# Performance work log

Measured on AMD Instinct MI355X. Metric: run time of the kernel, lower is better.

The kernel has to match this reference:

```python
import jax, jax.numpy as jnp
import numpy as np

B, S, D, H = 2, 2048, 1024, 16
DK = D // H
THETA = 10000.0


def _freqs_cos_sin(dim, seq_len, theta=THETA):
    # matches precompute_freqs_cis: freqs over full d_model, pairs of adjacent dims
    inv = 1.0 / theta ** (np.arange(0, dim, 2)[: dim // 2].astype(np.float32) / dim)
    t = np.arange(seq_len, dtype=np.float32)
    ang = np.outer(t, inv)  # [S, D/2]
    return jnp.asarray(np.cos(ang)), jnp.asarray(np.sin(ang))


def setup_inputs() -> dict:
    key = jax.random.key(0)
    ks = jax.random.split(key, 11)
    sc = 1.0 / np.sqrt(D)
    cos, sin = _freqs_cos_sin(D, S)
    return {
        "query": jax.random.normal(ks[0], (B, S, D), jnp.float32),
        "key": jax.random.normal(ks[1], (B, S, D), jnp.float32),
        "value": jax.random.normal(ks[2], (B, S, D), jnp.float32),
        "wq": jax.random.normal(ks[3], (D, D), jnp.float32) * sc,
        "bq": jnp.zeros((D,), jnp.float32),
        "wk": jax.random.normal(ks[4], (D, D), jnp.float32) * sc,
        "bk": jnp.zeros((D,), jnp.float32),
        "wv": jax.random.normal(ks[5], (D, D), jnp.float32) * sc,
        "bv": jnp.zeros((D,), jnp.float32),
        "wo": jax.random.normal(ks[6], (D, D), jnp.float32) * sc,
        "bo": jnp.zeros((D,), jnp.float32),
        "cos": cos,  # [S, D/2]
        "sin": sin,  # [S, D/2]
    }


def _rope(x, cos, sin):
    # x: [B,S,D]; pairs are adjacent elements along D (view_as_complex semantics)
    xr = x.reshape(*x.shape[:-1], -1, 2)  # [B,S,D/2,2]
    x0, x1 = xr[..., 0], xr[..., 1]
    c, s = cos[None], sin[None]  # broadcast over batch
    o0 = x0 * c - x1 * s
    o1 = x0 * s + x1 * c
    return jnp.stack([o0, o1], axis=-1).reshape(x.shape)


def reference(query, key, value, wq, bq, wk, bk, wv, bv, wo, bo, cos, sin):
    q = query @ wq.T + bq
    k = key @ wk.T + bk
    v = value @ wv.T + bv
    q = _rope(q, cos, sin)
    k = _rope(k, cos, sin)
    # split heads: [B,S,D] -> [B,H,S,DK]
    q = q.reshape(B, S, H, DK).transpose(0, 2, 1, 3)
    k = k.reshape(B, S, H, DK).transpose(0, 2, 1, 3)
    v = v.reshape(B, S, H, DK).transpose(0, 2, 1, 3)
    scores = jnp.einsum("bhqd,bhkd->bhqk", q, k) / jnp.sqrt(jnp.float32(DK))
    attn = jax.nn.softmax(scores, axis=-1)  # dropout is identity in eval
    out = jnp.einsum("bhqk,bhkd->bhqd", attn, v)
    out = out.transpose(0, 2, 1, 3).reshape(B, S, D)
    return out @ wo.T + bo
```

## Files before the change

kernel.cpp:

```cpp
#include <hip/hip_runtime.h>
#include <hip/hip_fp16.h>

typedef _Float16 f16;
using f16x8 = __attribute__((ext_vector_type(8))) _Float16;
using h2 = __attribute__((ext_vector_type(2))) __fp16;
using f32x4 = __attribute__((ext_vector_type(4))) float;
using f32x16 = __attribute__((ext_vector_type(16))) float;

#define LOG2E 1.4426950408889634f

__device__ __forceinline__ void gload16(const void* g, void* l) {
  __builtin_amdgcn_global_load_lds(
      (const __attribute__((address_space(1))) void*)g,
      (__attribute__((address_space(3))) void*)l, 16, 0, 0);
}

__device__ __forceinline__ float b32(h2 x) { return __builtin_bit_cast(float, x); }
__device__ __forceinline__ unsigned u32(h2 x) { return __builtin_bit_cast(unsigned, x); }

__global__ __launch_bounds__(256) void convert_k(
    const float* __restrict__ q, const float* __restrict__ k, const float* __restrict__ v,
    const float* __restrict__ wq, const float* __restrict__ wk,
    const float* __restrict__ wv, const float* __restrict__ wo,
    f16* __restrict__ dst) {
  const size_t SEG = (size_t)4 * 1024 * 1024;
  size_t i = ((size_t)blockIdx.x * 256 + threadIdx.x) * 8;
  const float* src; size_t off;
  if (i < SEG)            { src = q;  off = i; }
  else if (i < 2 * SEG)   { src = k;  off = i - SEG; }
  else if (i < 3 * SEG)   { src = v;  off = i - 2 * SEG; }
  else {
    size_t wi = i - 3 * SEG;
    int s = (int)(wi >> 20);
    src = (s == 0) ? wq : (s == 1) ? wk : (s == 2) ? wv : wo;
    off = wi & ((1u << 20) - 1);
  }
  float4 a = *(const float4*)(src + off);
  float4 b = *(const float4*)(src + off + 4);
  f16x8 o;
  o[0] = (f16)a.x; o[1] = (f16)a.y; o[2] = (f16)a.z; o[3] = (f16)a.w;
  o[4] = (f16)b.x; o[5] = (f16)b.y; o[6] = (f16)b.z; o[7] = (f16)b.w;
  *(f16x8*)(dst + i) = o;
}

template <int QKV>
__global__ __launch_bounds__(256) void gemm_k(
    const f16* __restrict__ Abase, const f16* __restrict__ Wbase,
    const float* __restrict__ b0, const float* __restrict__ b1, const float* __restrict__ b2,
    const float* __restrict__ cosT, const float* __restrict__ sinT,
    f16* __restrict__ qh, f16* __restrict__ kh, f16* __restrict__ vt,
    float* __restrict__ outF) {
  __shared__ f16 As[2][128 * 32];
  __shared__ f16 Bs[2][128 * 32];
  int tid = threadIdx.x, wid = tid >> 6, lane = tid & 63;
  int z = QKV ? blockIdx.z : 0;
  const f16* A = Abase + (size_t)z * (4u * 1024 * 1024);
  const f16* W = Wbase + (size_t)z * (1024u * 1024);
  int m0 = blockIdx.y * 128, n0 = blockIdx.x * 128;
  int wr = wid >> 1, wc = wid & 1;
  f32x4 acc[4][4] = {};

  int srow = tid >> 2;
  int sslot = (tid & 3) ^ (srow & 3);
  const f16* asrc0 = A + (size_t)(m0 + srow) * 1024 + sslot * 8;
  const f16* asrc1 = A + (size_t)(m0 + 64 + srow) * 1024 + sslot * 8;
  const f16* bsrc0 = W + (size_t)(n0 + srow) * 1024 + sslot * 8;
  const f16* bsrc1 = W + (size_t)(n0 + 64 + srow) * 1024 + sslot * 8;

  int aoff[4], boff[4];
#pragma unroll
  for (int i = 0; i < 4; ++i) {
    int row = wr * 64 + i * 16 + (lane & 15);
    aoff[i] = row * 32 + (((lane >> 4) ^ (row & 3)) * 8);
    int col = wc * 64 + i * 16 + (lane & 15);
    boff[i] = col * 32 + (((lane >> 4) ^ (col & 3)) * 8);
  }

  gload16(asrc0, (void*)(&As[0][0] + wid * 512));
  gload16(asrc1, (void*)(&As[0][0] + 2048 + wid * 512));
  gload16(bsrc0, (void*)(&Bs[0][0] + wid * 512));
  gload16(bsrc1, (void*)(&Bs[0][0] + 2048 + wid * 512));
  __syncthreads();

  int cur = 0;
  for (int kt = 0; kt < 32; ++kt) {
    if (kt + 1 < 32) {
      int k0 = (kt + 1) * 32;
      gload16(asrc0 + k0, (void*)(&As[cur ^ 1][0] + wid * 512));
      gload16(asrc1 + k0, (void*)(&As[cur ^ 1][0] + 2048 + wid * 512));
      gload16(bsrc0 + k0, (void*)(&Bs[cur ^ 1][0] + wid * 512));
      gload16(bsrc1 + k0, (void*)(&Bs[cur ^ 1][0] + 2048 + wid * 512));
    }
    f16x8 af[4], bf[4];
#pragma unroll
    for (int i = 0; i < 4; ++i) {
      af[i] = *(const f16x8*)(&As[cur][0] + aoff[i]);
      bf[i] = *(const f16x8*)(&Bs[cur][0] + boff[i]);
    }
#pragma unroll
    for (int i = 0; i < 4; ++i)
#pragma unroll
      for (int j = 0; j < 4; ++j)
        acc[i][j] = __builtin_amdgcn_mfma_f32_16x16x32_f16(af[i], bf[j], acc[i][j], 0, 0, 0);
    __syncthreads();
    cur ^= 1;
  }

  const float* bias = QKV ? (z == 0 ? b0 : (z == 1 ? b1 : b2)) : b0;
#pragma unroll
  for (int i = 0; i < 4; ++i) {
#pragma unroll
    for (int j = 0; j < 4; ++j) {
#pragma unroll
      for (int r = 0; r < 4; ++r) {
        int grow = m0 + wr * 64 + i * 16 + ((lane >> 4) << 2) + r;
        int gcol = n0 + wc * 64 + j * 16 + (lane & 15);
        float val = acc[i][j][r] + bias[gcol];
        if (QKV) {
          int s = grow & 2047, bb = grow >> 11;
          int h = gcol >> 6, dk = gcol & 63;
          if (z < 2) {
            float pr = __shfl_xor(val, 1);
            int j2 = gcol >> 1;
            float c = cosT[s * 512 + j2], sn = sinT[s * 512 + j2];
            val = (lane & 1) ? (c * val + sn * pr) : (c * val - sn * pr);
            if (z == 0) val *= 0.125f * LOG2E;
            f16* dst = (z == 0) ? qh : kh;
            dst[(((size_t)bb * 16 + h) * 2048 + s) * 64 + dk] = (f16)val;
          } else {
            vt[(((size_t)bb * 16 + h) * 64 + dk) * 2048 + s] = (f16)val;
          }
        } else {
          outF[(size_t)grow * 1024 + gcol] = val;
        }
      }
    }
  }
}

__global__ __launch_bounds__(256, 4) void flash_k(
    const f16* __restrict__ qh, const f16* __restrict__ kh, const f16* __restrict__ vt,
    f16* __restrict__ op, float2* __restrict__ mlbuf) {
  __shared__ f16 Ks[2][64 * 64];
  __shared__ f16 Vs[2][64 * 64];
  int tid = threadIdx.x, wid = tid >> 6, lane = tid & 63;
  int l31 = lane & 31, hi = lane >> 5;
  int qt = blockIdx.x, h = blockIdx.y, z = blockIdx.z;
  int b = z >> 1, ks = z & 1;
  size_t bh = (size_t)b * 16 + h;
  const f16* qp = qh + bh * (2048 * 64);
  const f16* kp = kh + bh * (2048 * 64) + (size_t)ks * 1024 * 64;
  const f16* vp = vt + bh * (64 * 2048) + ks * 1024;
  int qrow = qt * 128 + wid * 32 + l31;

  f16x8 qf[4];
#pragma unroll
  for (int kk = 0; kk < 4; ++kk)
    qf[kk] = *(const f16x8*)(qp + (size_t)qrow * 64 + kk * 16 + hi * 8);

  int srowA = tid >> 3, srowB = srowA + 32;
  int schA = (tid & 7) ^ (srowA & 7);
  int schB = (tid & 7) ^ (srowB & 7);
  const f16* ksrcA = kp + (size_t)srowA * 64 + schA * 8;
  const f16* ksrcB = kp + (size_t)srowB * 64 + schB * 8;
  const f16* vsrcA = vp + (size_t)srowA * 2048 + schA * 8;
  const f16* vsrcB = vp + (size_t)srowB * 2048 + schB * 8;

  int offr[2][4];
#pragma unroll
  for (int kb = 0; kb < 2; ++kb)
#pragma unroll
    for (int kk = 0; kk < 4; ++kk) {
      int row = kb * 32 + l31;
      offr[kb][kk] = (row * 128 + kk * 32 + hi * 16) ^ ((row & 7) << 4);
    }

  float m_ = -1e30f, l_ = 0.f;
  f32x16 oacc[2] = {};

  gload16(ksrcA, (char*)&Ks[0][0] + tid * 16);
  gload16(ksrcB, (char*)&Ks[0][0] + 4096 + tid * 16);
  gload16(vsrcA, (char*)&Vs[0][0] + tid * 16);
  gload16(vsrcB, (char*)&Vs[0][0] + 4096 + tid * 16);
  __syncthreads();

  int cur = 0;
  for (int kt = 0; kt < 16; ++kt) {
    if (kt + 1 < 16) {
      gload16(ksrcA + (size_t)(kt + 1) * 4096, (char*)&Ks[cur ^ 1][0] + tid * 16);
      gload16(ksrcB + (size_t)(kt + 1) * 4096, (char*)&Ks[cur ^ 1][0] + 4096 + tid * 16);
      gload16(vsrcA + (size_t)(kt + 1) * 64, (char*)&Vs[cur ^ 1][0] + tid * 16);
      gload16(vsrcB + (size_t)(kt + 1) * 64, (char*)&Vs[cur ^ 1][0] + 4096 + tid * 16);
    }

    const char* kbase = (const char*)&Ks[cur][0];
    f32x16 sacc[2] = {};
#pragma unroll
    for (int kb = 0; kb < 2; ++kb)
#pragma unroll
      for (int kk = 0; kk < 4; ++kk) {
        f16x8 af = *(const f16x8*)(kbase + offr[kb][kk]);
        sacc[kb] = __builtin_amdgcn_mfma_f32_32x32x16_f16(af, qf[kk], sacc[kb], 0, 0, 0);
      }

    float t16[16];
#pragma unroll
    for (int i = 0; i < 16; ++i) t16[i] = fmaxf(sacc[0][i], sacc[1][i]);
#pragma unroll
    for (int s = 8; s; s >>= 1)
#pragma unroll
      for (int i = 0; i < s; ++i) t16[i] = fmaxf(t16[i], t16[i + s]);
    float pmax = fmaxf(t16[0], __shfl_xor(t16[0], 32));

    if (!__all(pmax <= m_ + 8.0f)) {
      float mn = fmaxf(m_, pmax);
      float al = __builtin_amdgcn_exp2f(m_ - mn);
      m_ = mn;
      l_ *= al;
#pragma unroll
      for (int mb = 0; mb < 2; ++mb)
#pragma unroll
        for (int i = 0; i < 16; ++i) oacc[mb][i] *= al;
    }

#pragma unroll
    for (int kb = 0; kb < 2; ++kb)
#pragma unroll
      for (int i = 0; i < 16; ++i)
        sacc[kb][i] = __builtin_amdgcn_exp2f(sacc[kb][i] - m_);
#pragma unroll
    for (int i = 0; i < 16; ++i) t16[i] = sacc[0][i] + sacc[1][i];
#pragma unroll
    for (int s = 8; s; s >>= 1)
#pragma unroll
      for (int i = 0; i < s; ++i) t16[i] += t16[i + s];
    l_ += t16[0] + __shfl_xor(t16[0], 32);

    f16x8 pa[4];
#pragma unroll
    for (int kk = 0; kk < 4; ++kk) {
      int kb = kk >> 1, c8 = (kk & 1) * 8;
      float wA = b32(__builtin_amdgcn_cvt_pkrtz(sacc[kb][c8 + 0], sacc[kb][c8 + 1]));
      float wB = b32(__builtin_amdgcn_cvt_pkrtz(sacc[kb][c8 + 2], sacc[kb][c8 + 3]));
      float wC = b32(__builtin_amdgcn_cvt_pkrtz(sacc[kb][c8 + 4], sacc[kb][c8 + 5]));
      float wD = b32(__builtin_amdgcn_cvt_pkrtz(sacc[kb][c8 + 6], sacc[kb][c8 + 7]));
      float oA = __shfl_xor(wA, 32), oB = __shfl_xor(wB, 32);
      float oC = __shfl_xor(wC, 32), oD = __shfl_xor(wD, 32);
      float4 ff;
      ff.x = hi ? oC : wA;
      ff.y = hi ? oD : wB;
      ff.z = hi ? wC : oA;
      ff.w = hi ? wD : oB;
      pa[kk] = __builtin_bit_cast(f16x8, ff);
    }

    const char* vbase = (const char*)&Vs[cur][0];
#pragma unroll
    for (int kk = 0; kk < 4; ++kk)
#pragma unroll
      for (int mb = 0; mb < 2; ++mb) {
        f16x8 av = *(const f16x8*)(vbase + offr[mb][kk]);
        oacc[mb] = __builtin_amdgcn_mfma_f32_32x32x16_f16(av, pa[kk], oacc[mb], 0, 0, 0);
      }

    __syncthreads();
    cur ^= 1;
  }

  float inv = 1.f / l_;
  f16* orow = op + (((size_t)z * 16 + h) * 2048 + qrow) * 64;
#pragma unroll
  for (int mb = 0; mb < 2; ++mb)
#pragma unroll
    for (int g = 0; g < 4; ++g) {
      uint2 st;
      st.x = u32(__builtin_amdgcn_cvt_pkrtz(oacc[mb][4 * g + 0] * inv, oacc[mb][4 * g + 1] * inv));
      st.y = u32(__builtin_amdgcn_cvt_pkrtz(oacc[mb][4 * g + 2] * inv, oacc[mb][4 * g + 3] * inv));
      *(uint2*)(orow + mb * 32 + g * 8 + hi * 4) = st;
    }
  if (hi == 0)
    mlbuf[((size_t)z * 16 + h) * 2048 + qrow] = make_float2(m_, l_);
}

__global__ __launch_bounds__(256) void combine_k(
    const f16* __restrict__ op, const float2* __restrict__ ml, f16* __restrict__ attnout) {
  int t = blockIdx.x * 256 + threadIdx.x;
  int row = t >> 3, c8 = t & 7;
  int b = row >> 15, h = (row >> 11) & 15, qrow = row & 2047;
  size_t i0 = ((size_t)(b * 2 + 0) * 16 + h) * 2048 + qrow;
  size_t i1 = ((size_t)(b * 2 + 1) * 16 + h) * 2048 + qrow;
  float2 a = ml[i0], c = ml[i1];
  float M = fmaxf(a.x, c.x);
  float w1 = a.y * __builtin_amdgcn_exp2f(a.x - M);
  float w2 = c.y * __builtin_amdgcn_exp2f(c.x - M);
  float inv = 1.f / (w1 + w2);
  w1 *= inv; w2 *= inv;
  f16x8 o1 = *(const f16x8*)(op + i0 * 64 + c8 * 8);
  f16x8 o2 = *(const f16x8*)(op + i1 * 64 + c8 * 8);
  f16x8 o;
#pragma unroll
  for (int e = 0; e < 8; ++e)
    o[e] = (f16)(w1 * (float)o1[e] + w2 * (float)o2[e]);
  *(f16x8*)(attnout + ((size_t)b * 2048 + qrow) * 1024 + h * 64 + c8 * 8) = o;
}

extern "C" void kernel_launch(void* const* d_in, const int* in_sizes, int n_in,
                              void* d_out, int out_size, void* d_ws, size_t ws_size,
                              hipStream_t stream) {
  (void)in_sizes; (void)n_in; (void)out_size; (void)ws_size;
  const float* query = (const float*)d_in[0];
  const float* key   = (const float*)d_in[1];
  const float* value = (const float*)d_in[2];
  const float* wq = (const float*)d_in[3];
  const float* bq = (const float*)d_in[4];
  const float* wk = (const float*)d_in[5];
  const float* bk = (const float*)d_in[6];
  const float* wv = (const float*)d_in[7];
  const float* bv = (const float*)d_in[8];
  const float* wo = (const float*)d_in[9];
  const float* bo = (const float*)d_in[10];
  const float* cosT = (const float*)d_in[11];
  const float* sinT = (const float*)d_in[12];
  float* out = (float*)d_out;
  f16* ws = (f16*)d_ws;
  const size_t SEG = (size_t)4 * 1024 * 1024;
  f16* Xh = ws;
  f16* Wh = ws + 3 * SEG;
  f16* qh = ws + 16u * 1024 * 1024;
  f16* kh = qh + SEG;
  f16* vt = kh + SEG;
  f16* attnout = ws;
  f16* op = ws + SEG;
  float2* mlb = (float2*)(ws + 12u * 1024 * 1024);

  convert_k<<<8192, 256, 0, stream>>>(query, key, value, wq, wk, wv, wo, ws);
  gemm_k<1><<<dim3(8, 32, 3), 256, 0, stream>>>(Xh, Wh, bq, bk, bv, cosT, sinT,
                                                qh, kh, vt, nullptr);
  flash_k<<<dim3(16, 16, 4), 256, 0, stream>>>(qh, kh, vt, op, mlb);
  combine_k<<<2048, 256, 0, stream>>>(op, mlb, attnout);
  gemm_k<0><<<dim3(8, 32, 1), 256, 0, stream>>>(attnout, Wh + 3u * 1024 * 1024, bo,
                                                nullptr, nullptr, nullptr, nullptr,
                                                nullptr, nullptr, nullptr, out);
}
```

Before: 170.4 us.

## Stage QKV GEMM epilogue through LDS for coalesced stores and remap blocks per XCD

The QKV epilogue now writes the rotated, biased fp16 results into a swizzled shared-memory tile, then writes whole 16-byte rows for Q/K and transposed 16-byte runs for V^T, in place of the old scattered 2-byte stores. Block indices are also remapped so that consecutive blocks on each XCD share nearby row tiles, aiming for better L2 reuse of A and W. The two staging buffers are merged into one array so the tile can be reused for the epilogue. This adds an extra barrier and LDS traffic, and the remap assumes the grid is 8 wide by 32 tall.

```diff
diff --git a/kernel.cpp b/kernel.cpp
--- a/kernel.cpp
+++ b/kernel.cpp
@@ -50,13 +50,16 @@
     const float* __restrict__ cosT, const float* __restrict__ sinT,
     f16* __restrict__ qh, f16* __restrict__ kh, f16* __restrict__ vt,
     float* __restrict__ outF) {
-  __shared__ f16 As[2][128 * 32];
-  __shared__ f16 Bs[2][128 * 32];
+  __shared__ f16 sm[4][128 * 32];
   int tid = threadIdx.x, wid = tid >> 6, lane = tid & 63;
   int z = QKV ? blockIdx.z : 0;
   const f16* A = Abase + (size_t)z * (4u * 1024 * 1024);
   const f16* W = Wbase + (size_t)z * (1024u * 1024);
-  int m0 = blockIdx.y * 128, n0 = blockIdx.x * 128;
+
+  int lid = blockIdx.x + (blockIdx.y << 3);
+  int xcd = lid & 7, q = lid >> 3;
+  int m0 = (xcd * 4 + (q & 3)) * 128;
+  int n0 = (q >> 2) * 128;
   int wr = wid >> 1, wc = wid & 1;
   f32x4 acc[4][4] = {};
 
@@ -76,26 +79,26 @@
     boff[i] = col * 32 + (((lane >> 4) ^ (col & 3)) * 8);
   }
 
-  gload16(asrc0, (void*)(&As[0][0] + wid * 512));
-  gload16(asrc1, (void*)(&As[0][0] + 2048 + wid * 512));
-  gload16(bsrc0, (void*)(&Bs[0][0] + wid * 512));
-  gload16(bsrc1, (void*)(&Bs[0][0] + 2048 + wid * 512));
+  gload16(asrc0, (void*)(&sm[0][0] + wid * 512));
+  gload16(asrc1, (void*)(&sm[0][0] + 2048 + wid * 512));
+  gload16(bsrc0, (void*)(&sm[2][0] + wid * 512));
+  gload16(bsrc1, (void*)(&sm[2][0] + 2048 + wid * 512));
   __syncthreads();
 
   int cur = 0;
   for (int kt = 0; kt < 32; ++kt) {
     if (kt + 1 < 32) {
       int k0 = (kt + 1) * 32;
-      gload16(asrc0 + k0, (void*)(&As[cur ^ 1][0] + wid * 512));
-      gload16(asrc1 + k0, (void*)(&As[cur ^ 1][0] + 2048 + wid * 512));
-      gload16(bsrc0 + k0, (void*)(&Bs[cur ^ 1][0] + wid * 512));
-      gload16(bsrc1 + k0, (void*)(&Bs[cur ^ 1][0] + 2048 + wid * 512));
+      gload16(asrc0 + k0, (void*)(&sm[cur ^ 1][0] + wid * 512));
+      gload16(asrc1 + k0, (void*)(&sm[cur ^ 1][0] + 2048 + wid * 512));
+      gload16(bsrc0 + k0, (void*)(&sm[2 + (cur ^ 1)][0] + wid * 512));
+      gload16(bsrc1 + k0, (void*)(&sm[2 + (cur ^ 1)][0] + 2048 + wid * 512));
     }
     f16x8 af[4], bf[4];
 #pragma unroll
     for (int i = 0; i < 4; ++i) {
-      af[i] = *(const f16x8*)(&As[cur][0] + aoff[i]);
-      bf[i] = *(const f16x8*)(&Bs[cur][0] + boff[i]);
+      af[i] = *(const f16x8*)(&sm[cur][0] + aoff[i]);
+      bf[i] = *(const f16x8*)(&sm[2 + cur][0] + boff[i]);
     }
 #pragma unroll
     for (int i = 0; i < 4; ++i)
@@ -107,31 +110,69 @@
   }
 
   const float* bias = QKV ? (z == 0 ? b0 : (z == 1 ? b1 : b2)) : b0;
-#pragma unroll
-  for (int i = 0; i < 4; ++i) {
-#pragma unroll
-    for (int j = 0; j < 4; ++j) {
-#pragma unroll
-      for (int r = 0; r < 4; ++r) {
-        int grow = m0 + wr * 64 + i * 16 + ((lane >> 4) << 2) + r;
-        int gcol = n0 + wc * 64 + j * 16 + (lane & 15);
-        float val = acc[i][j][r] + bias[gcol];
-        if (QKV) {
-          int s = grow & 2047, bb = grow >> 11;
-          int h = gcol >> 6, dk = gcol & 63;
+
+  if (QKV) {
+    f16* Ct = &sm[0][0];
+#pragma unroll
+    for (int i = 0; i < 4; ++i) {
+#pragma unroll
+      for (int j = 0; j < 4; ++j) {
+#pragma unroll
+        for (int r = 0; r < 4; ++r) {
+          int row_l = wr * 64 + i * 16 + ((lane >> 4) << 2) + r;
+          int col_l = wc * 64 + j * 16 + (lane & 15);
+          int gcol = n0 + col_l;
+          float val = acc[i][j][r] + bias[gcol];
           if (z < 2) {
+            int s = (m0 + row_l) & 2047;
             float pr = __shfl_xor(val, 1);
             int j2 = gcol >> 1;
             float c = cosT[s * 512 + j2], sn = sinT[s * 512 + j2];
             val = (lane & 1) ? (c * val + sn * pr) : (c * val - sn * pr);
             if (z == 0) val *= 0.125f * LOG2E;
-            f16* dst = (z == 0) ? qh : kh;
-            dst[(((size_t)bb * 16 + h) * 2048 + s) * 64 + dk] = (f16)val;
-          } else {
-            vt[(((size_t)bb * 16 + h) * 64 + dk) * 2048 + s] = (f16)val;
           }
-        } else {
-          outF[(size_t)grow * 1024 + gcol] = val;
+          Ct[row_l * 128 + (col_l ^ ((row_l & 7) << 3))] = (f16)val;
+        }
+      }
+    }
+    __syncthreads();
+    int bb = m0 >> 11, sbase = m0 & 2047;
+    if (z < 2) {
+      int row = tid >> 1, halfsel = tid & 1;
+      int h = (n0 >> 6) + halfsel;
+      f16* dst = (z == 0 ? qh : kh) +
+                 (((size_t)bb * 16 + h) * 2048 + sbase + row) * 64;
+#pragma unroll
+      for (int ch = 0; ch < 8; ++ch) {
+        int c = halfsel * 64 + ch * 8;
+        f16x8 v = *(const f16x8*)(Ct + row * 128 + (c ^ ((row & 7) << 3)));
+        *(f16x8*)(dst + ch * 8) = v;
+      }
+    } else {
+      int c = tid & 127, halfsel = tid >> 7;
+      int h = (n0 >> 6) + (c >> 6), dk = c & 63;
+      f16* dst = vt + (((size_t)bb * 16 + h) * 64 + dk) * 2048 + sbase + halfsel * 64;
+#pragma unroll
+      for (int g = 0; g < 8; ++g) {
+        f16x8 v;
+#pragma unroll
+        for (int e = 0; e < 8; ++e) {
+          int r = halfsel * 64 + g * 8 + e;
+          v[e] = Ct[r * 128 + (c ^ ((r & 7) << 3))];
+        }
+        *(f16x8*)(dst + g * 8) = v;
+      }
+    }
+  } else {
+#pragma unroll
+    for (int i = 0; i < 4; ++i) {
+#pragma unroll
+      for (int j = 0; j < 4; ++j) {
+#pragma unroll
+        for (int r = 0; r < 4; ++r) {
+          int grow = m0 + wr * 64 + i * 16 + ((lane >> 4) << 2) + r;
+          int gcol = n0 + wc * 64 + j * 16 + (lane & 15);
+          outF[(size_t)grow * 1024 + gcol] = acc[i][j][r] + bias[gcol];
         }
       }
     }
```

After: 158.0 us. 7.3% less time.
